# Kernel optimization log

Measured on AMD Instinct MI355X. Metric: run time of the kernel, lower is better.

The kernel has to match this reference:

```python
import jax, jax.numpy as jnp
import numpy as np

B, S, HID = 2, 2048, 1024
H, D = 16, 64
NUM_BUCKETS, MAX_DIST = 32, 128
NEG_INF = -1e9


def _rel_buckets(rel_pos, num_buckets, max_distance):
    # decoder (unidirectional): only non-positive relative positions valid
    rp = -jnp.minimum(rel_pos, 0)  # [q,k] >= 0
    max_exact = num_buckets // 2
    is_small = rp < max_exact
    safe = jnp.maximum(rp, 1).astype(jnp.float32)
    large = max_exact + (
        jnp.log(safe / max_exact) / np.log(max_distance / max_exact) * (num_buckets - max_exact)
    ).astype(jnp.int32)
    large = jnp.minimum(large, num_buckets - 1)
    return jnp.where(is_small, rp, large)


def _rotate_half(t):
    t1, t2 = jnp.split(t, 2, axis=-1)
    return jnp.concatenate([-t2, t1], axis=-1)


def setup_inputs() -> dict:
    key = jax.random.key(0)
    ks = jax.random.split(key, 6)
    sc = 0.02
    x = jax.random.normal(ks[0], (B, S, HID), jnp.float32)
    Wq = jax.random.normal(ks[1], (HID, H * D), jnp.float32) * sc
    Wk = jax.random.normal(ks[2], (HID, H * D), jnp.float32) * sc
    Wv = jax.random.normal(ks[3], (HID, H * D), jnp.float32) * sc
    Wo = jax.random.normal(ks[4], (H * D, HID), jnp.float32) * sc
    rel_bias = jax.random.normal(ks[5], (NUM_BUCKETS, H), jnp.float32) * sc
    # rotary tables: emb = cat(freqs, freqs), non-interleave layout
    inv_freq = 1.0 / (10000.0 ** (np.arange(0, D, 2, dtype=np.float32) / D))
    freqs = np.arange(S, dtype=np.float32)[:, None] * inv_freq[None, :]  # [S, D/2]
    emb = np.concatenate([freqs, freqs], axis=-1)  # [S, D]
    cos = jnp.asarray(np.cos(emb), jnp.float32)
    sin = jnp.asarray(np.sin(emb), jnp.float32)
    return {"x": x, "Wq": Wq, "Wk": Wk, "Wv": Wv, "Wo": Wo,
            "rel_bias": rel_bias, "cos": cos, "sin": sin}


def reference(x, Wq, Wk, Wv, Wo, rel_bias, cos, sin):
    # QKV projections (weights stored [in, out])
    q = (x @ Wq).reshape(B, S, H, D)
    k = (x @ Wk).reshape(B, S, H, D)
    v = (x @ Wv).reshape(B, S, H, D)
    # RoPE (non-interleave): q*cos + rotate_half(q)*sin, cos/sin broadcast over B,H
    c = cos[None, :, None, :]
    s = sin[None, :, None, :]
    q = q * c + _rotate_half(q) * s
    k = k * c + _rotate_half(k) * s
    # scores [B,H,S,S]
    scores = jnp.einsum("bqhd,bkhd->bhqk", q, k) / np.sqrt(D).astype(np.float32)
    # learned relative-position bucket bias (T5-style, decoder/unidirectional)
    ctx_pos = jnp.arange(S)[:, None]
    mem_pos = jnp.arange(S)[None, :]
    buckets = _rel_buckets(mem_pos - ctx_pos, NUM_BUCKETS, MAX_DIST)  # [S,S]
    bias = rel_bias[buckets]  # [S,S,H]
    scores = scores + jnp.transpose(bias, (2, 0, 1))[None]
    # causal mask (decoder self-attention)
    causal = mem_pos <= ctx_pos  # [S,S]
    scores = jnp.where(causal[None, None], scores, NEG_INF)
    attn = jax.nn.softmax(scores, axis=-1)
    ctx = jnp.einsum("bhqk,bkhd->bqhd", attn, v).reshape(B, S, H * D)
    return ctx @ Wo
```

## Files before the change

### kernel.cpp

```cpp
#include <hip/hip_runtime.h>
#include <hip/hip_bf16.h>
#include <math.h>

#define B_   2
#define S_   2048
#define HID_ 1024
#define H_   16
#define D_   64
#define HD_  (H_ * D_)

typedef __attribute__((ext_vector_type(8))) short bf16x8;
typedef __attribute__((ext_vector_type(4))) short bf16x4;
typedef __attribute__((ext_vector_type(4))) float f32x4;
typedef __attribute__((ext_vector_type(4))) unsigned uint4v;
typedef unsigned short u16;

#define LOG2E 1.44269504088896f

static __device__ __forceinline__ u16 f2bf(float f) {
    unsigned u = __builtin_bit_cast(unsigned, f);
    u += 0x7fffu + ((u >> 16) & 1u);
    return (u16)(u >> 16);
}
static __device__ __forceinline__ unsigned cvtpk(float lo, float hi) {
    unsigned r;
    asm("v_cvt_pk_bf16_f32 %0, %1, %2" : "=v"(r) : "v"(lo), "v"(hi));
    return r;
}
static __device__ __forceinline__ int swzK(int row, int colbytes) {
    return row * 128 + (colbytes ^ ((row & 7) << 4));
}
static __device__ __forceinline__ int swzV(int row, int colbytes) {
    return row * 128 + (colbytes ^ ((row & 7) << 4) ^ (((row >> 3) & 1) << 3));
}
static __device__ __forceinline__ void gll16(const void* g, void* l) {
    __builtin_amdgcn_global_load_lds(
        (const __attribute__((address_space(1))) unsigned int*)g,
        (__attribute__((address_space(3))) unsigned int*)l, 16, 0, 0);
}

__global__ __launch_bounds__(256) void prep(const float* __restrict__ x,
                                            u16* __restrict__ xb,
                                            const float* __restrict__ W0,
                                            const float* __restrict__ W1,
                                            const float* __restrict__ W2,
                                            const float* __restrict__ W3,
                                            u16* __restrict__ o0,
                                            u16* __restrict__ o1,
                                            u16* __restrict__ o2,
                                            u16* __restrict__ o3) {
    __shared__ float tS[32][33];
    const int bid = blockIdx.x;
    if (bid < 4096) {
        int i = bid * 256 + threadIdx.x;
        float4 f = ((const float4*)x)[i];
        ushort4 u;
        u.x = f2bf(f.x); u.y = f2bf(f.y); u.z = f2bf(f.z); u.w = f2bf(f.w);
        ((ushort4*)xb)[i] = u;
    } else {
        const int id  = bid - 4096;
        const int z   = id >> 10;
        const int rem = id & 1023;
        const float* in = z == 0 ? W0 : z == 1 ? W1 : z == 2 ? W2 : W3;
        u16* out       = z == 0 ? o0 : z == 1 ? o1 : z == 2 ? o2 : o3;
        const int bx = (rem & 31) * 32, by = (rem >> 5) * 32;
        const int xx = threadIdx.x & 31, yy = threadIdx.x >> 5;
        #pragma unroll
        for (int j = 0; j < 4; j++)
            tS[yy + j * 8][xx] = in[(long)(by + yy + j * 8) * HID_ + bx + xx];
        __syncthreads();
        #pragma unroll
        for (int j = 0; j < 4; j++)
            out[(long)(bx + yy + j * 8) * HID_ + by + xx] = f2bf(tS[xx][yy + j * 8]);
    }
}

__global__ __launch_bounds__(256, 3) void gemm_qkv(const u16* __restrict__ A,
                                                   const u16* __restrict__ Bt,
                                                   u16* __restrict__ outb,
                                                   const float* __restrict__ cosb,
                                                   const float* __restrict__ sinb,
                                                   int K) {
    __shared__ u16 As[128 * 64];
    __shared__ u16 Bs[128 * 64];
    const int t = threadIdx.x;
    const int lane = t & 63;
    const int w = t >> 6;
    const int qlane = lane & 15, grp = lane >> 4;
    const int m0 = blockIdx.y * 128, n0 = blockIdx.x * 128;
    const int wr = w >> 1, wc = w & 1;

    f32x4 acc[4][4];
    #pragma unroll
    for (int i = 0; i < 4; i++)
        #pragma unroll
        for (int j = 0; j < 4; j++) acc[i][j] = (f32x4){0.f, 0.f, 0.f, 0.f};

    const int srow = lane >> 3;
    const int scol = ((lane & 7) ^ srow) * 8;
    const int swa  = (qlane & 7) << 4;
    const int nkt = K >> 6;
    for (int kt = 0; kt < nkt; kt++) {
        const int k0 = kt << 6;
        #pragma unroll
        for (int c = 0; c < 4; c++) {
            const int chunk = w * 4 + c;
            const int row = chunk * 8 + srow;
            gll16(A  + (long)(m0 + row) * K + k0 + scol, As + chunk * 512);
            gll16(Bt + (long)(n0 + row) * K + k0 + scol, Bs + chunk * 512);
        }
        __syncthreads();
        #pragma unroll
        for (int ks = 0; ks < 2; ks++) {
            bf16x8 af[4], bfr[4];
            #pragma unroll
            for (int i = 0; i < 4; i++) {
                af[i]  = *(const bf16x8*)((const unsigned char*)As
                         + (wr * 64 + i * 16 + qlane) * 128 + ((ks * 64 + grp * 16) ^ swa));
                bfr[i] = *(const bf16x8*)((const unsigned char*)Bs
                         + (wc * 64 + i * 16 + qlane) * 128 + ((ks * 64 + grp * 16) ^ swa));
            }
            #pragma unroll
            for (int mf = 0; mf < 4; mf++)
                #pragma unroll
                for (int nf = 0; nf < 4; nf++)
                    acc[mf][nf] = __builtin_amdgcn_mfma_f32_16x16x32_bf16(bfr[nf], af[mf], acc[mf][nf], 0, 0, 0);
        }
        __syncthreads();
    }

    const int gnb = n0 + wc * 64;
    const bool isqk = gnb < 2048;
    const bool isq  = gnb < 1024;
    const float QS = 0.125f * LOG2E;
    #pragma unroll
    for (int mf = 0; mf < 4; mf++) {
        const int m = m0 + wr * 64 + mf * 16 + qlane;
        if (isqk) {
            const int s = m & (S_ - 1);
            const float* cr = cosb + s * 64;
            const float* sr = sinb + s * 64;
            #pragma unroll
            for (int nf2 = 0; nf2 < 2; nf2++) {
                #pragma unroll
                for (int r = 0; r < 4; r++) {
                    const int d = nf2 * 16 + grp * 4 + r;
                    float lo = acc[mf][nf2][r], hi = acc[mf][nf2 + 2][r];
                    float nlo = lo * cr[d]      - hi * sr[d];
                    float nhi = hi * cr[d + 32] + lo * sr[d + 32];
                    if (isq) { nlo *= QS; nhi *= QS; }
                    acc[mf][nf2][r]     = nlo;
                    acc[mf][nf2 + 2][r] = nhi;
                }
            }
        }
        #pragma unroll
        for (int nf = 0; nf < 4; nf++) {
            const int gn = gnb + nf * 16 + grp * 4;
            ushort4 o4;
            o4.x = f2bf(acc[mf][nf][0]); o4.y = f2bf(acc[mf][nf][1]);
            o4.z = f2bf(acc[mf][nf][2]); o4.w = f2bf(acc[mf][nf][3]);
            *(ushort4*)&outb[((long)(gn >> 10)) * ((long)4096 * 1024) + (long)m * 1024 + (gn & 1023)] = o4;
        }
    }
}

__global__ __launch_bounds__(256, 3) void gemm_n64(const u16* __restrict__ A,
                                                   const u16* __restrict__ Bt,
                                                   float* __restrict__ outf,
                                                   int K) {
    __shared__ u16 As[128 * 32];
    __shared__ u16 Bs[64 * 32];
    const int t = threadIdx.x;
    const int lane = t & 63;
    const int w = t >> 6;
    const int qlane = lane & 15, grp = lane >> 4;
    const int m0 = blockIdx.y * 128, n0 = blockIdx.x * 64;

    f32x4 acc[2][4];
    #pragma unroll
    for (int i = 0; i < 2; i++)
        #pragma unroll
        for (int j = 0; j < 4; j++) acc[i][j] = (f32x4){0.f, 0.f, 0.f, 0.f};

    const int srow = (lane >> 2);
    const int scol = (lane & 3) * 8;
    const int nkt = K >> 5;
    for (int kt = 0; kt < nkt; kt++) {
        const int k0 = kt << 5;
        #pragma unroll
        for (int c = 0; c < 2; c++) {
            const int chunk = w * 2 + c;
            const int row = chunk * 16 + srow;
            gll16(A + (long)(m0 + row) * K + k0 + scol, As + chunk * 512);
        }
        gll16(Bt + (long)(n0 + w * 16 + srow) * K + k0 + scol, Bs + w * 512);
        __syncthreads();
        bf16x8 af[2], bfr[4];
        #pragma unroll
        for (int i = 0; i < 2; i++)
            af[i] = *(const bf16x8*)(As + (w * 32 + i * 16 + qlane) * 32 + grp * 8);
        #pragma unroll
        for (int i = 0; i < 4; i++)
            bfr[i] = *(const bf16x8*)(Bs + (i * 16 + qlane) * 32 + grp * 8);
        #pragma unroll
        for (int mf = 0; mf < 2; mf++)
            #pragma unroll
            for (int nf = 0; nf < 4; nf++)
                acc[mf][nf] = __builtin_amdgcn_mfma_f32_16x16x32_bf16(bfr[nf], af[mf], acc[mf][nf], 0, 0, 0);
        __syncthreads();
    }

    #pragma unroll
    for (int mf = 0; mf < 2; mf++) {
        const int m = m0 + w * 32 + mf * 16 + qlane;
        #pragma unroll
        for (int nf = 0; nf < 4; nf++) {
            float4 o4;
            o4.x = acc[mf][nf][0]; o4.y = acc[mf][nf][1];
            o4.z = acc[mf][nf][2]; o4.w = acc[mf][nf][3];
            *(float4*)&outf[(long)m * 1024 + n0 + nf * 16 + grp * 4] = o4;
        }
    }
}

__global__ __launch_bounds__(512, 4) void attn_mfma(const u16* __restrict__ q,
                                                    const u16* __restrict__ k,
                                                    const u16* __restrict__ v,
                                                    const float* __restrict__ rel_bias,
                                                    u16* __restrict__ ctx) {
    __shared__ __align__(16) unsigned char kS[2][8192];
    __shared__ __align__(16) unsigned char vS[2][8192];
    __shared__ float bb[2][192];

    const int t    = threadIdx.x;
    const int lane = t & 63;
    const int w    = t >> 6;
    const int n    = blockIdx.x;
    const int xcd  = n & 7;
    const int hbhi = (n >> 7) & 3;
    int qtb        = (n >> 3) & 15;
    if (hbhi & 2) qtb = 15 - qtb;
    const int hb   = xcd + (hbhi << 3);
    const int h    = hb & 15, b = hb >> 4;
    const int q0   = qtb * 128;
    const int wq   = w * 16;
    const int qwq  = q0 + wq;
    const int qlane = lane & 15;
    const int grp   = lane >> 4;

    const long bhbase = ((long)b * S_ * H_ + h) * D_;
    const float bfar  = rel_bias[31 * H_ + h] * LOG2E;

    const int krow8 = lane >> 3;
    const int kcsw  = ((lane & 7) ^ krow8) * 8;
    const u16* kpw  = k + bhbase + (long)(w * 8 + krow8) * HD_ + kcsw;
    const int vrb = (t >> 5) * 4,  vcp = (t & 31) * 2;

    bf16x8 qf0, qf1;
    {
        const u16* qrow = q + bhbase + (long)(qwq + qlane) * HD_;
        qf0 = *(const bf16x8*)(qrow + grp * 8);
        qf1 = *(const bf16x8*)(qrow + 32 + grp * 8);
    }

    f32x4 oacc[4];
    #pragma unroll
    for (int db = 0; db < 4; db++) oacc[db] = (f32x4){0.f, 0.f, 0.f, 0.f};
    float m_run = -1.0e30f, l_run = 0.f;

    unsigned vreg[4];
    float breg = 0.f;

    auto stageK = [&](int k0, int buf) {
        gll16(kpw + (long)k0 * HD_, kS[buf] + w * 1024);
    };
    auto prefetch = [&](int k0, bool needb) {
        const u16* vp = v + bhbase + (long)(k0 + vrb) * HD_ + vcp;
        #pragma unroll
        for (int i = 0; i < 4; i++)
            vreg[i] = *(const unsigned*)(vp + (long)i * HD_);
        if (needb && t < 192) {
            int rp = (q0 - 63) + t - k0;
            float bv = 0.f;
            if (rp >= 0) {
                int bucket;
                if (rp < 16) bucket = rp;
                else {
                    int lg = (int)(logf((float)rp * 0.0625f) * 7.69437361f);
                    bucket = 16 + lg;
                    if (bucket > 31) bucket = 31;
                }
                bv = rel_bias[bucket * H_ + h] * LOG2E;
            }
            breg = bv;
        }
    };
    auto writetile = [&](int buf, bool needb) {
        ushort2 a0 = __builtin_bit_cast(ushort2, vreg[0]);
        ushort2 a1 = __builtin_bit_cast(ushort2, vreg[1]);
        ushort2 a2 = __builtin_bit_cast(ushort2, vreg[2]);
        ushort2 a3 = __builtin_bit_cast(ushort2, vreg[3]);
        ushort4 d0; d0.x = a0.x; d0.y = a1.x; d0.z = a2.x; d0.w = a3.x;
        ushort4 d1; d1.x = a0.y; d1.y = a1.y; d1.z = a2.y; d1.w = a3.y;
        *(ushort4*)(vS[buf] + swzV(vcp,     vrb * 2)) = d0;
        *(ushort4*)(vS[buf] + swzV(vcp + 1, vrb * 2)) = d1;
        if (needb && t < 192) bb[buf][t] = breg;
    };

    const int NT = 2 * qtb + 2;
    const bool needb0 = (q0 < 176);
    stageK(0, 0);
    prefetch(0, needb0);
    writetile(0, needb0);
    __syncthreads();

    int cur = 0;
    for (int kt = 0; kt < NT; kt++) {
        const int k0 = kt * 64;
        const bool has_next = (kt + 1) < NT;
        const bool needb_n  = (q0 - (k0 + 64)) < 176;
        if (has_next) {
            stageK(k0 + 64, cur ^ 1);
            prefetch(k0 + 64, needb_n);
        }

        const bool skip = k0 > qwq + 15;
        if (!skip) {
            const bool use_bias = (qwq - k0) < 176;
            const bool is_diag  = (k0 + 63) > qwq;

            __builtin_amdgcn_s_setprio(1);
            f32x4 sacc[4];
            #pragma unroll
            for (int kb = 0; kb < 4; kb++) {
                sacc[kb] = (f32x4){0.f, 0.f, 0.f, 0.f};
                bf16x8 kf0 = *(const bf16x8*)(kS[cur] + swzK(kb * 16 + qlane, grp * 16));
                bf16x8 kf1 = *(const bf16x8*)(kS[cur] + swzK(kb * 16 + qlane, 64 + grp * 16));
                sacc[kb] = __builtin_amdgcn_mfma_f32_16x16x32_bf16(kf0, qf0, sacc[kb], 0, 0, 0);
                sacc[kb] = __builtin_amdgcn_mfma_f32_16x16x32_bf16(kf1, qf1, sacc[kb], 0, 0, 0);
            }
            __builtin_amdgcn_s_setprio(0);

            float pv_[4][4];
            float tmax = -1.0e30f;
            #pragma unroll
            for (int kb = 0; kb < 4; kb++) {
                #pragma unroll
                for (int r = 0; r < 4; r++) {
                    float s = sacc[kb][r];
                    if (use_bias) {
                        const int k_l = kb * 16 + grp * 4 + r;
                        s += bb[cur][wq + qlane - k_l + 63];
                        if (is_diag)
                            s = ((k0 + k_l) <= (qwq + qlane)) ? s : -1.0e9f;
                    }
                    pv_[kb][r] = s;
                }
                tmax = fmaxf(tmax,
                       fmaxf(fmaxf(pv_[kb][0], pv_[kb][1]), fmaxf(pv_[kb][2], pv_[kb][3])));
            }
            tmax = fmaxf(tmax, __shfl_xor(tmax, 16));
            tmax = fmaxf(tmax, __shfl_xor(tmax, 32));

            const float bofs = use_bias ? 0.f : bfar;
            const float teff = tmax + bofs;
            float msub;
            if (__all(teff <= m_run + 11.5f)) {
                msub = m_run - bofs;
            } else {
                float mnew  = fmaxf(m_run, teff);
                float scale = __builtin_amdgcn_exp2f(m_run - mnew);
                l_run *= scale;
                #pragma unroll
                for (int db = 0; db < 4; db++)
                    #pragma unroll
                    for (int r = 0; r < 4; r++) oacc[db][r] *= scale;
                m_run = mnew;
                msub = mnew - bofs;
            }

            float tsum = 0.f;
            #pragma unroll
            for (int kb = 0; kb < 4; kb++)
                #pragma unroll
                for (int r = 0; r < 4; r++) {
                    float p = __builtin_amdgcn_exp2f(pv_[kb][r] - msub);
                    pv_[kb][r] = p;
                    tsum += p;
                }
            tsum += __shfl_xor(tsum, 16);
            tsum += __shfl_xor(tsum, 32);
            l_run += tsum;

            bf16x8 pf[2];
            #pragma unroll
            for (int ks = 0; ks < 2; ks++) {
                unsigned u0 = cvtpk(pv_[2 * ks][0], pv_[2 * ks][1]);
                unsigned u1 = cvtpk(pv_[2 * ks][2], pv_[2 * ks][3]);
                unsigned u2 = cvtpk(pv_[2 * ks + 1][0], pv_[2 * ks + 1][1]);
                unsigned u3 = cvtpk(pv_[2 * ks + 1][2], pv_[2 * ks + 1][3]);
                pf[ks] = __builtin_bit_cast(bf16x8, (uint4v){u0, u1, u2, u3});
            }

            __builtin_amdgcn_s_setprio(1);
            #pragma unroll
            for (int db = 0; db < 4; db++) {
                #pragma unroll
                for (int ks = 0; ks < 2; ks++) {
                    bf16x4 lo = *(const bf16x4*)(vS[cur] + swzV(db * 16 + qlane, ks * 64 + grp * 8));
                    bf16x4 hi = *(const bf16x4*)(vS[cur] + swzV(db * 16 + qlane, ks * 64 + 32 + grp * 8));
                    bf16x8 vf = __builtin_shufflevector(lo, hi, 0, 1, 2, 3, 4, 5, 6, 7);
                    oacc[db] = __builtin_amdgcn_mfma_f32_16x16x32_bf16(vf, pf[ks], oacc[db], 0, 0, 0);
                }
            }
            __builtin_amdgcn_s_setprio(0);
        }

        if (has_next) writetile(cur ^ 1, needb_n);
        __syncthreads();
        cur ^= 1;
    }

    const float inv = 1.0f / l_run;
    u16* dst = ctx + (long)(b * S_ + qwq + qlane) * HID_ + h * D_;
    #pragma unroll
    for (int db = 0; db < 4; db++) {
        ushort4 o4;
        o4.x = f2bf(oacc[db][0] * inv);
        o4.y = f2bf(oacc[db][1] * inv);
        o4.z = f2bf(oacc[db][2] * inv);
        o4.w = f2bf(oacc[db][3] * inv);
        *(ushort4*)(dst + db * 16 + grp * 4) = o4;
    }
}

extern "C" void kernel_launch(void* const* d_in, const int* in_sizes, int n_in,
                              void* d_out, int out_size, void* d_ws, size_t ws_size,
                              hipStream_t stream) {
    const float* x    = (const float*)d_in[0];
    const float* Wq   = (const float*)d_in[1];
    const float* Wk   = (const float*)d_in[2];
    const float* Wv   = (const float*)d_in[3];
    const float* Wo   = (const float*)d_in[4];
    const float* rb   = (const float*)d_in[5];
    const float* cosb = (const float*)d_in[6];
    const float* sinb = (const float*)d_in[7];
    float* out = (float*)d_out;

    char* wsb = (char*)d_ws;
    u16* xb    = (u16*)(wsb);
    u16* wqkvT = (u16*)(wsb + (8L  << 20));
    u16* woT   = (u16*)(wsb + (14L << 20));
    u16* qb    = (u16*)(wsb + (16L << 20));
    u16* kb    = (u16*)(wsb + (24L << 20));
    u16* vb    = (u16*)(wsb + (32L << 20));
    u16* ctxb  = (u16*)(wsb + (40L << 20));

    hipLaunchKernelGGL(prep, dim3(4096 + 4096), dim3(256), 0, stream,
                       x, xb, Wq, Wk, Wv, Wo,
                       wqkvT, wqkvT + (1L << 20), wqkvT + (2L << 20), woT);
    hipLaunchKernelGGL(gemm_qkv, dim3(24, 32), dim3(256), 0, stream,
                       xb, wqkvT, qb, cosb, sinb, HID_);
    hipLaunchKernelGGL(attn_mfma, dim3(512), dim3(512), 0, stream,
                       qb, kb, vb, rb, ctxb);
    hipLaunchKernelGGL(gemm_n64, dim3(16, 32), dim3(256), 0, stream,
                       ctxb, woT, out, HID_);
}
```

Baseline: 126.2 us.

## Widen output GEMM K-tile to 64 with swizzled LDS; register-stage K in attention

The output-projection GEMM now loads 64-wide K tiles per iteration into an XOR-swizzled shared-memory layout and runs two MFMA substeps per tile. This halves the number of barrier pairs and is meant to avoid LDS bank conflicts on the fragment reads. The attention kernel stops using direct global-to-LDS loads for K. Instead it prefetches K into registers along with V and writes it into the swizzled LDS buffer during the tile write. This uses more LDS in the GEMM, which may lower occupancy, and more registers in attention.

```diff
diff --git a/kernel.cpp b/kernel.cpp
--- a/kernel.cpp
+++ b/kernel.cpp
@@ -169,8 +169,8 @@
                                                    const u16* __restrict__ Bt,
                                                    float* __restrict__ outf,
                                                    int K) {
-    __shared__ u16 As[128 * 32];
-    __shared__ u16 Bs[64 * 32];
+    __shared__ u16 As[128 * 64];
+    __shared__ u16 Bs[64 * 64];
     const int t = threadIdx.x;
     const int lane = t & 63;
     const int w = t >> 6;
@@ -183,31 +183,40 @@
         #pragma unroll
         for (int j = 0; j < 4; j++) acc[i][j] = (f32x4){0.f, 0.f, 0.f, 0.f};
 
-    const int srow = (lane >> 2);
-    const int scol = (lane & 3) * 8;
-    const int nkt = K >> 5;
+    const int srow = lane >> 3;
+    const int scol = ((lane & 7) ^ srow) * 8;
+    const int swa  = (qlane & 7) << 4;
+    const int nkt = K >> 6;
     for (int kt = 0; kt < nkt; kt++) {
-        const int k0 = kt << 5;
+        const int k0 = kt << 6;
+        #pragma unroll
+        for (int c = 0; c < 4; c++) {
+            const int chunk = w * 4 + c;
+            gll16(A + (long)(m0 + chunk * 8 + srow) * K + k0 + scol, As + chunk * 512);
+        }
         #pragma unroll
         for (int c = 0; c < 2; c++) {
             const int chunk = w * 2 + c;
-            const int row = chunk * 16 + srow;
-            gll16(A + (long)(m0 + row) * K + k0 + scol, As + chunk * 512);
-        }
-        gll16(Bt + (long)(n0 + w * 16 + srow) * K + k0 + scol, Bs + w * 512);
-        __syncthreads();
-        bf16x8 af[2], bfr[4];
-        #pragma unroll
-        for (int i = 0; i < 2; i++)
-            af[i] = *(const bf16x8*)(As + (w * 32 + i * 16 + qlane) * 32 + grp * 8);
-        #pragma unroll
-        for (int i = 0; i < 4; i++)
-            bfr[i] = *(const bf16x8*)(Bs + (i * 16 + qlane) * 32 + grp * 8);
-        #pragma unroll
-        for (int mf = 0; mf < 2; mf++)
-            #pragma unroll
-            for (int nf = 0; nf < 4; nf++)
-                acc[mf][nf] = __builtin_amdgcn_mfma_f32_16x16x32_bf16(bfr[nf], af[mf], acc[mf][nf], 0, 0, 0);
+            gll16(Bt + (long)(n0 + chunk * 8 + srow) * K + k0 + scol, Bs + chunk * 512);
+        }
+        __syncthreads();
+        #pragma unroll
+        for (int ks = 0; ks < 2; ks++) {
+            bf16x8 af[2], bfr[4];
+            #pragma unroll
+            for (int i = 0; i < 2; i++)
+                af[i] = *(const bf16x8*)((const unsigned char*)As
+                        + (w * 32 + i * 16 + qlane) * 128 + ((ks * 64 + grp * 16) ^ swa));
+            #pragma unroll
+            for (int i = 0; i < 4; i++)
+                bfr[i] = *(const bf16x8*)((const unsigned char*)Bs
+                         + (i * 16 + qlane) * 128 + ((ks * 64 + grp * 16) ^ swa));
+            #pragma unroll
+            for (int mf = 0; mf < 2; mf++)
+                #pragma unroll
+                for (int nf = 0; nf < 4; nf++)
+                    acc[mf][nf] = __builtin_amdgcn_mfma_f32_16x16x32_bf16(bfr[nf], af[mf], acc[mf][nf], 0, 0, 0);
+        }
         __syncthreads();
     }
 
@@ -252,9 +261,7 @@
     const long bhbase = ((long)b * S_ * H_ + h) * D_;
     const float bfar  = rel_bias[31 * H_ + h] * LOG2E;
 
-    const int krow8 = lane >> 3;
-    const int kcsw  = ((lane & 7) ^ krow8) * 8;
-    const u16* kpw  = k + bhbase + (long)(w * 8 + krow8) * HD_ + kcsw;
+    const int kr  = t >> 3,        kc  = (t & 7) * 8;
     const int vrb = (t >> 5) * 4,  vcp = (t & 31) * 2;
 
     bf16x8 qf0, qf1;
@@ -269,13 +276,12 @@
     for (int db = 0; db < 4; db++) oacc[db] = (f32x4){0.f, 0.f, 0.f, 0.f};
     float m_run = -1.0e30f, l_run = 0.f;
 
+    bf16x8 kreg;
     unsigned vreg[4];
     float breg = 0.f;
 
-    auto stageK = [&](int k0, int buf) {
-        gll16(kpw + (long)k0 * HD_, kS[buf] + w * 1024);
-    };
     auto prefetch = [&](int k0, bool needb) {
+        kreg = *(const bf16x8*)(k + bhbase + (long)(k0 + kr) * HD_ + kc);
         const u16* vp = v + bhbase + (long)(k0 + vrb) * HD_ + vcp;
         #pragma unroll
         for (int i = 0; i < 4; i++)
@@ -297,6 +303,7 @@
         }
     };
     auto writetile = [&](int buf, bool needb) {
+        *(bf16x8*)(kS[buf] + swzK(kr, kc * 2)) = kreg;
         ushort2 a0 = __builtin_bit_cast(ushort2, vreg[0]);
         ushort2 a1 = __builtin_bit_cast(ushort2, vreg[1]);
         ushort2 a2 = __builtin_bit_cast(ushort2, vreg[2]);
@@ -310,7 +317,6 @@
 
     const int NT = 2 * qtb + 2;
     const bool needb0 = (q0 < 176);
-    stageK(0, 0);
     prefetch(0, needb0);
     writetile(0, needb0);
     __syncthreads();
@@ -320,10 +326,7 @@
         const int k0 = kt * 64;
         const bool has_next = (kt + 1) < NT;
         const bool needb_n  = (q0 - (k0 + 64)) < 176;
-        if (has_next) {
-            stageK(k0 + 64, cur ^ 1);
-            prefetch(k0 + 64, needb_n);
-        }
+        if (has_next) prefetch(k0 + 64, needb_n);
 
         const bool skip = k0 > qwq + 15;
         if (!skip) {
```

After: 117.4 us, median of 3. -7.0%, faster.
